# Kernel tuning notes

Hardware: AMD Instinct MI355X
Metric: run time of the kernel (lower is better)

The kernel has to match this reference:

```python
import jax, jax.numpy as jnp
import numpy as np
import math

N = 8192  # transform size (power of 2, so extended_n == n, no padding)
BATCH = 8192


def setup_inputs() -> dict:
    key = jax.random.key(0)
    x = jax.random.normal(key, (BATCH, N), dtype=jnp.float32)
    return {"x": x}


def reference(x):
    # Fast Walsh-Hadamard transform via m = log2(n) butterfly stages.
    # Each stage's twiddle is [[1,1],[1,-1]]/sqrt(2), so the overall result
    # is H_n @ x / sqrt(n) (torch module folds the 1/sqrt(2) into each stage).
    B, n = x.shape
    m = int(math.log2(n))
    h = 1  # current butterfly half-block size
    y = x
    for _ in range(m):
        # view as (B, n/(2h), 2, h): pairs separated by stride h
        y = y.reshape(B, -1, 2, h)
        a = y[:, :, 0, :]
        b = y[:, :, 1, :]
        y = jnp.stack([a + b, a - b], axis=2)
        h *= 2
    y = y.reshape(B, n)
    scale = jnp.asarray(1.0 / math.sqrt(n), dtype=x.dtype)
    return y * scale
```

## Files before the change

### kernel.cpp

```cpp
#include <hip/hip_runtime.h>


static __device__ __forceinline__ void bfly(float4& a, float4& b) {
    float ax = a.x, ay = a.y, az = a.z, aw = a.w;
    a.x = ax + b.x; a.y = ay + b.y; a.z = az + b.z; a.w = aw + b.w;
    b.x = ax - b.x; b.y = ay - b.y; b.z = az - b.z; b.w = aw - b.w;
}

static __device__ __forceinline__ int swz(int q) { return q ^ ((q >> 3) & 7); }

__global__ __launch_bounds__(256) void wht8192_kernel(const float* __restrict__ in,
                                                      float* __restrict__ out) {
    __shared__ float4 lds[2048];
    const int t = threadIdx.x;
    const int l = t & 63;
    const int w = t >> 6;
    const size_t row = blockIdx.x;
    const float* __restrict__ rin  = in  + row * 8192;
    float* __restrict__       rout = out + row * 8192;

    float4 v[8];

    #pragma unroll
    for (int k = 0; k < 8; ++k)
        v[k] = *reinterpret_cast<const float4*>(rin + ((k << 10) | (t << 2)));

    #pragma unroll
    for (int k = 0; k < 8; ++k) {
        float4 a = v[k];
        float s0 = a.x + a.y, d0 = a.x - a.y;
        float s1 = a.z + a.w, d1 = a.z - a.w;
        v[k].x = s0 + s1; v[k].z = s0 - s1;
        v[k].y = d0 + d1; v[k].w = d0 - d1;
    }
    bfly(v[0], v[1]); bfly(v[2], v[3]); bfly(v[4], v[5]); bfly(v[6], v[7]);
    bfly(v[0], v[2]); bfly(v[1], v[3]); bfly(v[4], v[6]); bfly(v[5], v[7]);
    bfly(v[0], v[4]); bfly(v[1], v[5]); bfly(v[2], v[6]); bfly(v[3], v[7]);

    #pragma unroll
    for (int k = 0; k < 8; ++k)
        lds[swz((k << 8) | t)] = v[k];
    __syncthreads();

    #pragma unroll
    for (int j = 0; j < 8; ++j)
        v[j] = lds[swz((t << 3) | j)];

    bfly(v[0], v[1]); bfly(v[2], v[3]); bfly(v[4], v[5]); bfly(v[6], v[7]);
    bfly(v[0], v[2]); bfly(v[1], v[3]); bfly(v[4], v[6]); bfly(v[5], v[7]);
    bfly(v[0], v[4]); bfly(v[1], v[5]); bfly(v[2], v[6]); bfly(v[3], v[7]);

    #pragma unroll
    for (int j = 0; j < 8; ++j)
        lds[swz((t << 3) | j)] = v[j];
    __syncthreads();

    const int base3 = (w << 9) | ((l >> 5) << 8) | (((l >> 3) & 3) << 6) | (l & 7);
    #pragma unroll
    for (int m = 0; m < 8; ++m)
        v[m] = lds[swz(base3 | (m << 3))];

    bfly(v[0], v[1]); bfly(v[2], v[3]); bfly(v[4], v[5]); bfly(v[6], v[7]);
    bfly(v[0], v[2]); bfly(v[1], v[3]); bfly(v[4], v[6]); bfly(v[5], v[7]);
    bfly(v[0], v[4]); bfly(v[1], v[5]); bfly(v[2], v[6]); bfly(v[3], v[7]);

    #pragma unroll
    for (int m = 0; m < 8; ++m)
        lds[swz(base3 | (m << 3))] = v[m];
    __syncthreads();

    #pragma unroll
    for (int m = 0; m < 8; ++m)
        v[m] = lds[swz((w << 9) | (m << 6) | l)];

    bfly(v[0], v[1]); bfly(v[2], v[3]); bfly(v[4], v[5]); bfly(v[6], v[7]);
    bfly(v[0], v[2]); bfly(v[1], v[3]); bfly(v[4], v[6]); bfly(v[5], v[7]);

    const float s = 0.011048543456039806f;
    #pragma unroll
    for (int m = 0; m < 8; ++m) {
        float4 a = v[m];
        a.x *= s; a.y *= s; a.z *= s; a.w *= s;
        *reinterpret_cast<float4*>(rout + (((w << 9) | (m << 6) | l) << 2)) = a;
    }
}

extern "C" void kernel_launch(void* const* d_in, const int* in_sizes, int n_in,
                              void* d_out, int out_size, void* d_ws, size_t ws_size,
                              hipStream_t stream) {
    const float* x = (const float*)d_in[0];
    float* out = (float*)d_out;
    const int rows = out_size / 8192;
    hipLaunchKernelGGL(wht8192_kernel, dim3(rows), dim3(256), 0, stream, x, out);
}
```

Baseline: 103.5 us.

## Use 128 threads with 16 float4 per thread, cutting LDS passes from three to two

Restructures the 8192-point WHT so each of 128 threads holds 16 float4 registers. The transform now runs as radix-16×4 in registers plus two LDS exchange rounds instead of three, which removes one shared-memory round trip and one barrier. Global loads and stores become nontemporal, and the swizzle is adjusted for the new access pattern. The cost is higher register pressure per thread and fewer threads per block, which may hurt latency hiding in a kernel that is close to memory-bound.

```diff
diff --git a/kernel.cpp b/kernel.cpp
--- a/kernel.cpp
+++ b/kernel.cpp
@@ -1,87 +1,85 @@
 #include <hip/hip_runtime.h>
 
 
-static __device__ __forceinline__ void bfly(float4& a, float4& b) {
-    float ax = a.x, ay = a.y, az = a.z, aw = a.w;
-    a.x = ax + b.x; a.y = ay + b.y; a.z = az + b.z; a.w = aw + b.w;
-    b.x = ax - b.x; b.y = ay - b.y; b.z = az - b.z; b.w = aw - b.w;
+typedef float f32x4 __attribute__((ext_vector_type(4)));
+
+static __device__ __forceinline__ void bfly(f32x4& a, f32x4& b) {
+    f32x4 t = a;
+    a = t + b;
+    b = t - b;
 }
 
-static __device__ __forceinline__ int swz(int q) { return q ^ ((q >> 3) & 7); }
+static __device__ __forceinline__ int swz(int q) { return q ^ ((q >> 4) & 7); }
 
-__global__ __launch_bounds__(256) void wht8192_kernel(const float* __restrict__ in,
+__global__ __launch_bounds__(128) void wht8192_kernel(const float* __restrict__ in,
                                                       float* __restrict__ out) {
-    __shared__ float4 lds[2048];
+    __shared__ f32x4 lds[2048];
     const int t = threadIdx.x;
-    const int l = t & 63;
-    const int w = t >> 6;
     const size_t row = blockIdx.x;
     const float* __restrict__ rin  = in  + row * 8192;
     float* __restrict__       rout = out + row * 8192;
 
-    float4 v[8];
+    f32x4 v[16];
 
     #pragma unroll
-    for (int k = 0; k < 8; ++k)
-        v[k] = *reinterpret_cast<const float4*>(rin + ((k << 10) | (t << 2)));
+    for (int k = 0; k < 16; ++k)
+        v[k] = __builtin_nontemporal_load(
+            reinterpret_cast<const f32x4*>(rin + ((k << 9) | (t << 2))));
 
     #pragma unroll
-    for (int k = 0; k < 8; ++k) {
-        float4 a = v[k];
+    for (int k = 0; k < 16; ++k) {
+        f32x4 a = v[k];
         float s0 = a.x + a.y, d0 = a.x - a.y;
         float s1 = a.z + a.w, d1 = a.z - a.w;
         v[k].x = s0 + s1; v[k].z = s0 - s1;
         v[k].y = d0 + d1; v[k].w = d0 - d1;
     }
-    bfly(v[0], v[1]); bfly(v[2], v[3]); bfly(v[4], v[5]); bfly(v[6], v[7]);
-    bfly(v[0], v[2]); bfly(v[1], v[3]); bfly(v[4], v[6]); bfly(v[5], v[7]);
-    bfly(v[0], v[4]); bfly(v[1], v[5]); bfly(v[2], v[6]); bfly(v[3], v[7]);
+    #pragma unroll
+    for (int s = 1; s < 16; s <<= 1) {
+        #pragma unroll
+        for (int m = 0; m < 16; ++m)
+            if (!(m & s)) bfly(v[m], v[m | s]);
+    }
 
     #pragma unroll
-    for (int k = 0; k < 8; ++k)
-        lds[swz((k << 8) | t)] = v[k];
+    for (int k = 0; k < 16; ++k)
+        lds[swz((k << 7) | t)] = v[k];
     __syncthreads();
 
     #pragma unroll
-    for (int j = 0; j < 8; ++j)
-        v[j] = lds[swz((t << 3) | j)];
-
-    bfly(v[0], v[1]); bfly(v[2], v[3]); bfly(v[4], v[5]); bfly(v[6], v[7]);
-    bfly(v[0], v[2]); bfly(v[1], v[3]); bfly(v[4], v[6]); bfly(v[5], v[7]);
-    bfly(v[0], v[4]); bfly(v[1], v[5]); bfly(v[2], v[6]); bfly(v[3], v[7]);
+    for (int j = 0; j < 16; ++j)
+        v[j] = lds[swz((t << 4) | j)];
 
     #pragma unroll
-    for (int j = 0; j < 8; ++j)
-        lds[swz((t << 3) | j)] = v[j];
+    for (int s = 1; s < 16; s <<= 1) {
+        #pragma unroll
+        for (int m = 0; m < 16; ++m)
+            if (!(m & s)) bfly(v[m], v[m | s]);
+    }
+
+    #pragma unroll
+    for (int j = 0; j < 16; ++j)
+        lds[swz((t << 4) | j)] = v[j];
     __syncthreads();
 
-    const int base3 = (w << 9) | ((l >> 5) << 8) | (((l >> 3) & 3) << 6) | (l & 7);
+    const int base3 = ((t >> 4) << 7) | (t & 15);
     #pragma unroll
-    for (int m = 0; m < 8; ++m)
-        v[m] = lds[swz(base3 | (m << 3))];
-
-    bfly(v[0], v[1]); bfly(v[2], v[3]); bfly(v[4], v[5]); bfly(v[6], v[7]);
-    bfly(v[0], v[2]); bfly(v[1], v[3]); bfly(v[4], v[6]); bfly(v[5], v[7]);
-    bfly(v[0], v[4]); bfly(v[1], v[5]); bfly(v[2], v[6]); bfly(v[3], v[7]);
+    for (int m = 0; m < 16; ++m)
+        v[m] = lds[swz(base3 | ((m >> 3) << 10) | ((m & 7) << 4))];
 
     #pragma unroll
-    for (int m = 0; m < 8; ++m)
-        lds[swz(base3 | (m << 3))] = v[m];
-    __syncthreads();
+    for (int s = 1; s < 8; s <<= 1) {
+        #pragma unroll
+        for (int m = 0; m < 16; ++m)
+            if (!(m & s)) bfly(v[m], v[m | s]);
+    }
 
+    const float sc = 0.011048543456039806f;
     #pragma unroll
-    for (int m = 0; m < 8; ++m)
-        v[m] = lds[swz((w << 9) | (m << 6) | l)];
-
-    bfly(v[0], v[1]); bfly(v[2], v[3]); bfly(v[4], v[5]); bfly(v[6], v[7]);
-    bfly(v[0], v[2]); bfly(v[1], v[3]); bfly(v[4], v[6]); bfly(v[5], v[7]);
-
-    const float s = 0.011048543456039806f;
-    #pragma unroll
-    for (int m = 0; m < 8; ++m) {
-        float4 a = v[m];
-        a.x *= s; a.y *= s; a.z *= s; a.w *= s;
-        *reinterpret_cast<float4*>(rout + (((w << 9) | (m << 6) | l) << 2)) = a;
+    for (int m = 0; m < 16; ++m) {
+        f32x4 a = v[m] * sc;
+        const int q = base3 | ((m >> 3) << 10) | ((m & 7) << 4);
+        __builtin_nontemporal_store(a, reinterpret_cast<f32x4*>(rout + (q << 2)));
     }
 }
 
@@ -91,5 +89,5 @@
     const float* x = (const float*)d_in[0];
     float* out = (float*)d_out;
     const int rows = out_size / 8192;
-    hipLaunchKernelGGL(wht8192_kernel, dim3(rows), dim3(256), 0, stream, x, out);
+    hipLaunchKernelGGL(wht8192_kernel, dim3(rows), dim3(128), 0, stream, x, out);
 }
```

Result: faster. 94.24 us (-8.9%).
